# Kernel optimization log

Measured on AMD Instinct MI355X. Metric: run time of the kernel, lower is better.

## Reference

```python
import jax, jax.numpy as jnp
import numpy as np

DIM = 1024
HIDDEN = 2560  # multiple_of*(int(2*4*DIM/3)//multiple_of)
N_EXPERTS = 4
TOP_K = 2


def setup_inputs() -> dict:
    key = jax.random.key(0)
    ks = jax.random.split(key, 5)
    scale_d = 1.0 / np.sqrt(DIM)
    scale_h = 1.0 / np.sqrt(HIDDEN)
    x = jax.random.normal(ks[0], (8, 1024, DIM), dtype=jnp.float32)
    gate_w = jax.random.normal(ks[1], (N_EXPERTS, DIM), dtype=jnp.float32) * scale_d
    # torch Linear weight layout [out, in]; stacked over experts
    w1 = jax.random.normal(ks[2], (N_EXPERTS, HIDDEN, DIM), dtype=jnp.float32) * scale_d
    w3 = jax.random.normal(ks[3], (N_EXPERTS, HIDDEN, DIM), dtype=jnp.float32) * scale_d
    w2 = jax.random.normal(ks[4], (N_EXPERTS, DIM, HIDDEN), dtype=jnp.float32) * scale_h
    return {"x": x, "gate_w": gate_w, "w1": w1, "w2": w2, "w3": w3}


def reference(x, gate_w, w1, w2, w3):
    orig_shape = x.shape
    xf = x.reshape(-1, orig_shape[-1])  # [N, D]

    # gating: softmax -> top-k -> renormalize
    logits = jnp.einsum('nd,ed->ne', xf, gate_w)
    probs = jax.nn.softmax(logits, axis=-1)
    topk_w, topk_idx = jax.lax.top_k(probs, TOP_K)          # [N, K]
    topk_w = topk_w / jnp.sum(topk_w, axis=-1, keepdims=True)

    # per-token per-expert combine weight (0 if expert not selected)
    one_hot = jax.nn.one_hot(topk_idx, N_EXPERTS, dtype=xf.dtype)  # [N, K, E]
    comb = jnp.einsum('nk,nke->ne', topk_w, one_hot)               # [N, E]

    # dense per-expert SwiGLU FFN (4 experts), then weighted combine
    h1 = jnp.einsum('nd,ehd->neh', xf, w1)   # [N, E, H]
    h3 = jnp.einsum('nd,ehd->neh', xf, w3)
    h = jax.nn.silu(h1) * h3
    y = jnp.einsum('neh,edh->ned', h, w2)    # [N, E, D]
    out = jnp.einsum('ned,ne->nd', y, comb)  # [N, D]

    aux_loss = jnp.asarray(0.0, dtype=x.dtype)  # eval mode
    return out.reshape(orig_shape), aux_loss
```

## Files before the change

### kernel.cpp

```cpp
#include <hip/hip_runtime.h>

typedef unsigned short u16;
typedef unsigned int   u32;

#define DIM  1024
#define HID  2560
#define NTOK 8192
#define NEXP 4

#define BM 128
#define BN 128
#define BK 64

#define IDXCAP 16896

typedef __attribute__((ext_vector_type(8))) short bf16x8;
typedef __attribute__((ext_vector_type(4))) float f32x4;

__device__ __forceinline__ void async16(const void* g, void* l) {
  __builtin_amdgcn_global_load_lds((const __attribute__((address_space(1))) u32*)g,
                                   (__attribute__((address_space(3))) u32*)l,
                                   16, 0, 0);
}
__device__ __forceinline__ u16 f2bf(float f) {
  union { float f; u32 u; } c; c.f = f;
  u32 u = c.u;
  return (u16)((u + 0x7fffu + ((u >> 16) & 1u)) >> 16);
}
__device__ __forceinline__ ushort4 cvt4(float4 v) {
  ushort4 o; o.x = f2bf(v.x); o.y = f2bf(v.y); o.z = f2bf(v.z); o.w = f2bf(v.w);
  return o;
}

__global__ void zero_kernel(float* __restrict__ out, int n, int* __restrict__ rt) {
  int i = blockIdx.x * blockDim.x + threadIdx.x;
  if (i < 8) rt[i] = 0;
  int n4 = n >> 2;
  int stride = gridDim.x * blockDim.x;
  float4 z = {0.f, 0.f, 0.f, 0.f};
  for (int j = i; j < n4; j += stride) ((float4*)out)[j] = z;
  if (i == 0)
    for (int j = n4 << 2; j < n; ++j) out[j] = 0.f;
}

__global__ void cvt13_kernel(const float* __restrict__ w1, const float* __restrict__ w3,
                             u16* __restrict__ w1b, u16* __restrict__ w3b, int n4each) {
  int i = blockIdx.x * blockDim.x + threadIdx.x;
  if (i < n4each)
    ((ushort4*)w1b)[i] = cvt4(((const float4*)w1)[i]);
  else if (i < 2 * n4each)
    ((ushort4*)w3b)[i - n4each] = cvt4(((const float4*)w3)[i - n4each]);
}

__global__ void cvt2_kernel(const float* __restrict__ w2, u16* __restrict__ w2b, int n4) {
  int i = blockIdx.x * blockDim.x + threadIdx.x;
  if (i < n4) ((ushort4*)w2b)[i] = cvt4(((const float4*)w2)[i]);
}

__global__ void gate_kernel(const float* __restrict__ X, const float* __restrict__ GW,
                            float* __restrict__ comb, int* __restrict__ rt,
                            u16* __restrict__ Xb) {
  __shared__ int s_cnt[NEXP];
  if (threadIdx.x < NEXP) s_cnt[threadIdx.x] = 0;
  __syncthreads();

  int gtid = blockIdx.x * blockDim.x + threadIdx.x;
  int tok  = gtid >> 6;
  int lane = gtid & 63;

  const float4* xv = (const float4*)(X + (size_t)tok * DIM + lane * 16);
  float4 x0 = xv[0], x1 = xv[1], x2 = xv[2], x3 = xv[3];

  ushort4* xb = (ushort4*)(Xb + (size_t)tok * DIM + lane * 16);
  xb[0] = cvt4(x0); xb[1] = cvt4(x1); xb[2] = cvt4(x2); xb[3] = cvt4(x3);

  float acc[NEXP];
#pragma unroll
  for (int e = 0; e < NEXP; ++e) {
    const float4* gv = (const float4*)(GW + e * DIM + lane * 16);
    float4 g0 = gv[0], g1 = gv[1], g2 = gv[2], g3 = gv[3];
    float s;
    s  = x0.x * g0.x + x0.y * g0.y + x0.z * g0.z + x0.w * g0.w;
    s += x1.x * g1.x + x1.y * g1.y + x1.z * g1.z + x1.w * g1.w;
    s += x2.x * g2.x + x2.y * g2.y + x2.z * g2.z + x2.w * g2.w;
    s += x3.x * g3.x + x3.y * g3.y + x3.z * g3.z + x3.w * g3.w;
    acc[e] = s;
  }
#pragma unroll
  for (int off = 32; off > 0; off >>= 1) {
#pragma unroll
    for (int e = 0; e < NEXP; ++e) acc[e] += __shfl_xor(acc[e], off);
  }
  if (lane == 0) {
    int i1 = 0;
#pragma unroll
    for (int e = 1; e < NEXP; ++e) if (acc[e] > acc[i1]) i1 = e;
    int i2 = -1;
#pragma unroll
    for (int e = 0; e < NEXP; ++e) {
      if (e == i1) continue;
      if (i2 < 0 || acc[e] > acc[i2]) i2 = e;
    }
    float m  = acc[i1];
    float e1 = __expf(acc[i1] - m), e2 = __expf(acc[i2] - m);
    float inv = 1.f / (e1 + e2);
    float w[NEXP] = {0.f, 0.f, 0.f, 0.f};
    w[i1] = e1 * inv; w[i2] = e2 * inv;
#pragma unroll
    for (int e = 0; e < NEXP; ++e) comb[(size_t)tok * NEXP + e] = w[e];
    atomicAdd(&s_cnt[i1], 1);
    atomicAdd(&s_cnt[i2], 1);
  }
  __syncthreads();
  if (threadIdx.x < NEXP) atomicAdd(&rt[threadIdx.x], s_cnt[threadIdx.x]);
}

__global__ void scan_kernel(int* __restrict__ rt) {
  if (threadIdx.x == 0 && blockIdx.x == 0) {
    int b = 0;
#pragma unroll
    for (int e = 0; e < NEXP; ++e) {
      rt[8 + e] = b;
      b += (rt[e] + BM - 1) & ~(BM - 1);
    }
  }
}

__global__ void fill_kernel(const float* __restrict__ comb, int* __restrict__ rt,
                            int* __restrict__ idxpool) {
  int t    = blockIdx.x * blockDim.x + threadIdx.x;
  int lane = threadIdx.x & 63;
  float4 c = ((const float4*)comb)[t];
  float cv[NEXP] = {c.x, c.y, c.z, c.w};
#pragma unroll
  for (int e = 0; e < NEXP; ++e) {
    bool sel = cv[e] > 0.f;
    unsigned long long b = __ballot(sel);
    int cw = __popcll(b);
    int bp = 0;
    if (lane == 0 && cw) bp = atomicAdd(&rt[4 + e], cw);
    bp = __shfl(bp, 0);
    if (sel) {
      int off = __popcll(b & ((1ull << lane) - 1ull));
      idxpool[rt[8 + e] + bp + off] = t;
    }
  }
}


__global__ __launch_bounds__(256, 2) void ffn13_kernel(
    const u16* __restrict__ Xb, const u16* __restrict__ W1,
    const u16* __restrict__ W3, const float* __restrict__ combp,
    const int* __restrict__ idxpool, const int* __restrict__ rt,
    u16* __restrict__ Hpool) {
  const int e   = blockIdx.y >> 6;
  const int mb  = blockIdx.y & 63;
  const int cnt = rt[e];
  const int m0  = mb * BM;
  if (m0 >= cnt) return;
  const int rbase = rt[8 + e];
  const int n0    = blockIdx.x * BN;

  __shared__ __align__(16) u16 As [BM * BK];
  __shared__ __align__(16) u16 B1s[BN * BK];
  __shared__ __align__(16) u16 B3s[BN * BK];
  __shared__ float s_comb[BM];
  __shared__ int   s_idx [BM];

  const int tid  = threadIdx.x;
  const int wave = tid >> 6;
  const int lane = tid & 63;

  if (tid < BM) {
    int m = m0 + tid;
    int t = (m < cnt) ? idxpool[rbase + m] : 0;
    s_idx[tid]  = t;
    s_comb[tid] = combp[(size_t)t * NEXP + e];
  }
  __syncthreads();

  const u16* W1e = W1 + (size_t)e * HID * DIM;
  const u16* W3e = W3 + (size_t)e * HID * DIM;

  const int scc = (((tid & 7) ^ ((tid >> 3) & 7)) << 3);
  const int r0  = tid >> 3;
  const u16 *pA[4], *pB1[4], *pB3[4];
  int dsto[4];
#pragma unroll
  for (int q = 0; q < 4; ++q) {
    int row = r0 + 32 * q;
    pA[q]   = Xb  + (size_t)s_idx[row] * DIM + scc;
    pB1[q]  = W1e + (size_t)(n0 + row) * DIM + scc;
    pB3[q]  = W3e + (size_t)(n0 + row) * DIM + scc;
    dsto[q] = (tid + 256 * q) * 8;
  }

  const int wm = (wave >> 1) * 64, wn = (wave & 1) * 64;
  const int quad = lane >> 4, r = lane & 15;

  f32x4 acc1[4][4], acc3[4][4];
#pragma unroll
  for (int i = 0; i < 4; ++i)
#pragma unroll
    for (int j = 0; j < 4; ++j) {
      acc1[i][j] = (f32x4){0.f, 0.f, 0.f, 0.f};
      acc3[i][j] = (f32x4){0.f, 0.f, 0.f, 0.f};
    }

  for (int k0 = 0; k0 < DIM; k0 += BK) {
    __syncthreads();
#pragma unroll
    for (int q = 0; q < 4; ++q) { async16(pA[q],  &As [dsto[q]]); pA[q]  += BK; }
#pragma unroll
    for (int q = 0; q < 4; ++q) { async16(pB1[q], &B1s[dsto[q]]); pB1[q] += BK; }
#pragma unroll
    for (int q = 0; q < 4; ++q) { async16(pB3[q], &B3s[dsto[q]]); pB3[q] += BK; }
    __syncthreads();

#pragma unroll
    for (int s = 0; s < 2; ++s) {
      bf16x8 af[4], b1f[4], b3f[4];
#pragma unroll
      for (int i = 0; i < 4; ++i) {
        int row = wm + i * 16 + r;
        af[i] = *(const bf16x8*)&As[row * BK + ((((s << 2) + quad) ^ (row & 7)) << 3)];
      }
#pragma unroll
      for (int j = 0; j < 4; ++j) {
        int row = wn + j * 16 + r;
        int cc  = (((s << 2) + quad) ^ (row & 7)) << 3;
        b1f[j] = *(const bf16x8*)&B1s[row * BK + cc];
        b3f[j] = *(const bf16x8*)&B3s[row * BK + cc];
      }
#pragma unroll
      for (int i = 0; i < 4; ++i)
#pragma unroll
        for (int j = 0; j < 4; ++j) {
          acc1[i][j] = __builtin_amdgcn_mfma_f32_16x16x32_bf16(af[i], b1f[j], acc1[i][j], 0, 0, 0);
          acc3[i][j] = __builtin_amdgcn_mfma_f32_16x16x32_bf16(af[i], b3f[j], acc3[i][j], 0, 0, 0);
        }
    }
  }

#pragma unroll
  for (int i = 0; i < 4; ++i) {
    const int rowb = wm + i * 16 + quad * 4;
#pragma unroll
    for (int rr = 0; rr < 4; ++rr) {
      const float cw = s_comb[rowb + rr];
      u16* orow = Hpool + (size_t)(rbase + m0 + rowb + rr) * HID + n0 + wn + r;
#pragma unroll
      for (int j = 0; j < 4; ++j) {
        float v1v = acc1[i][j][rr];
        float v3v = acc3[i][j][rr];
        float sig = 1.f / (1.f + __expf(-v1v));
        orow[j * 16] = f2bf(cw * (v1v * sig * v3v));
      }
    }
  }
}

__global__ __launch_bounds__(256, 2) void ffn2_kernel(
    const u16* __restrict__ Hpool, const u16* __restrict__ W2b,
    const int* __restrict__ idxpool, const int* __restrict__ rt,
    float* __restrict__ Out) {
  const int e   = blockIdx.x >> 9;
  const int bid = blockIdx.x & 511;
  const int cnt = rt[e];
  const int Mb  = (cnt + BM - 1) >> 7;
  const int xcd = bid & 7;
  const int k   = bid >> 3;
  const int mb  = xcd * 8 + (k >> 3);
  const int nb  = k & 7;
  if (mb >= Mb) return;
  const int rbase = rt[8 + e];
  const int m0 = mb * BM;
  const int n0 = nb * BN;

  __shared__ __align__(16) u16 As[BM * BK];
  __shared__ __align__(16) u16 Bs[BN * BK];
  __shared__ int s_idx[BM];

  const int tid  = threadIdx.x;
  const int wave = tid >> 6;
  const int lane = tid & 63;

  if (tid < BM) {
    int m = m0 + tid;
    s_idx[tid] = (m < cnt) ? idxpool[rbase + m] : -1;
  }

  const int scc = (((tid & 7) ^ ((tid >> 3) & 7)) << 3);
  const int r0  = tid >> 3;
  const u16 *pa[4], *pb[4];
  int dsto[4];
#pragma unroll
  for (int q = 0; q < 4; ++q) {
    int row = r0 + 32 * q;
    pa[q]   = Hpool + (size_t)(rbase + m0 + row) * HID + scc;
    pb[q]   = W2b + ((size_t)e * DIM + n0 + row) * HID + scc;
    dsto[q] = (tid + 256 * q) * 8;
  }

  const int wm = (wave >> 1) * 64, wn = (wave & 1) * 64;
  const int quad = lane >> 4, r = lane & 15;

  f32x4 acc[4][4];
#pragma unroll
  for (int i = 0; i < 4; ++i)
#pragma unroll
    for (int j = 0; j < 4; ++j) acc[i][j] = (f32x4){0.f, 0.f, 0.f, 0.f};

  for (int k0 = 0; k0 < HID; k0 += BK) {
    __syncthreads();
#pragma unroll
    for (int q = 0; q < 4; ++q) { async16(pa[q], &As[dsto[q]]); pa[q] += BK; }
#pragma unroll
    for (int q = 0; q < 4; ++q) { async16(pb[q], &Bs[dsto[q]]); pb[q] += BK; }
    __syncthreads();

#pragma unroll
    for (int s = 0; s < 2; ++s) {
      bf16x8 af[4], bf[4];
#pragma unroll
      for (int i = 0; i < 4; ++i) {
        int row = wm + i * 16 + r;
        af[i] = *(const bf16x8*)&As[row * BK + ((((s << 2) + quad) ^ (row & 7)) << 3)];
      }
#pragma unroll
      for (int j = 0; j < 4; ++j) {
        int row = wn + j * 16 + r;
        bf[j] = *(const bf16x8*)&Bs[row * BK + ((((s << 2) + quad) ^ (row & 7)) << 3)];
      }
#pragma unroll
      for (int i = 0; i < 4; ++i)
#pragma unroll
        for (int j = 0; j < 4; ++j)
          acc[i][j] = __builtin_amdgcn_mfma_f32_16x16x32_bf16(af[i], bf[j], acc[i][j], 0, 0, 0);
    }
  }

#pragma unroll
  for (int i = 0; i < 4; ++i) {
    const int rowb = wm + i * 16 + quad * 4;
#pragma unroll
    for (int rr = 0; rr < 4; ++rr) {
      int t = s_idx[rowb + rr];
      if (t >= 0) {
        float* orow = Out + (size_t)t * DIM + n0 + wn + r;
#pragma unroll
        for (int j = 0; j < 4; ++j) unsafeAtomicAdd(&orow[j * 16], acc[i][j][rr]);
      }
    }
  }
}

__global__ void ws_marker_kernel(float* __restrict__ Out, float v) {
  if (threadIdx.x == 0 && blockIdx.x == 0) Out[0] = v;
}

extern "C" void kernel_launch(void* const* d_in, const int* in_sizes, int n_in,
                              void* d_out, int out_size, void* d_ws, size_t ws_size,
                              hipStream_t stream) {
  const float* x  = (const float*)d_in[0];
  const float* gw = (const float*)d_in[1];
  const float* w1 = (const float*)d_in[2];
  const float* w2 = (const float*)d_in[3];
  const float* w3 = (const float*)d_in[4];
  float* out = (float*)d_out;

  const size_t WELEMS = (size_t)NEXP * HID * DIM;
  const size_t WBYTES = WELEMS * sizeof(u16);
  char* ws = (char*)d_ws;
  float* comb    = (float*)ws;
  int*   rt      = (int*)(ws + 131072);
  int*   idxpool = (int*)(ws + 131072 + 128);
  u16*   w1b     = (u16*)(ws + 131072 + 128 + (size_t)IDXCAP * 4);
  u16*   w2b     = w1b;
  u16*   w3b     = w1b + WELEMS;
  u16*   Xb      = w3b + WELEMS;
  u16*   Hpool   = Xb + (size_t)NTOK * DIM;

  const size_t need = 131072 + 128 + (size_t)IDXCAP * 4 + 2 * WBYTES +
                      (size_t)NTOK * DIM * sizeof(u16) +
                      (size_t)IDXCAP * HID * sizeof(u16);
  if (ws_size < need) {
    float v = 5000.0f + (float)((ws_size >> 20) > 999 ? 999 : (ws_size >> 20));
    ws_marker_kernel<<<dim3(1), dim3(64), 0, stream>>>(out, v);
    return;
  }

  zero_kernel<<<dim3(2048), dim3(256), 0, stream>>>(out, out_size / 4, rt);

  gate_kernel<<<dim3(NTOK / 4), dim3(256), 0, stream>>>(x, gw, comb, rt, Xb);
  scan_kernel<<<dim3(1), dim3(64), 0, stream>>>(rt);
  fill_kernel<<<dim3(NTOK / 256), dim3(256), 0, stream>>>(comb, rt, idxpool);

  {
    int n4each = (int)(WELEMS / 4);
    cvt13_kernel<<<dim3((2 * n4each + 255) / 256), dim3(256), 0, stream>>>(
        w1, w3, w1b, w3b, n4each);
  }

  ffn13_kernel<<<dim3(HID / BN, 64 * NEXP), dim3(256), 0, stream>>>(
      Xb, w1b, w3b, comb, idxpool, rt, Hpool);

  {
    int n4 = (int)(WELEMS / 4);
    cvt2_kernel<<<dim3((n4 + 255) / 256), dim3(256), 0, stream>>>(w2, w2b, n4);
  }

  ffn2_kernel<<<dim3(512 * NEXP), dim3(256), 0, stream>>>(Hpool, w2b, idxpool, rt, out);
}
```

Measured before the change: 567.6 us.

## Fuse zeroing and scan into other kernels; compact ffn2 grid to active tiles

Moves the output zeroing into the gate kernel and the routing-counter reset into the w1/w3 conversion kernel. It replaces the scan kernel with an inline per-expert base computation, which removes two kernel launches. ffn2 becomes a grid-stride loop over only the tiles that are actually populated, so blocks that would exit early on empty tiles are no longer launched. Each thread now recomputes expert offsets, and tile ordering changes from the XCD-aware mapping to an mb-major order, which may affect L2 reuse.

Result: faster. 522.8 us (-7.9%).

```diff
diff --git a/kernel.cpp b/kernel.cpp
--- a/kernel.cpp
+++ b/kernel.cpp
@@ -31,20 +31,20 @@
   ushort4 o; o.x = f2bf(v.x); o.y = f2bf(v.y); o.z = f2bf(v.z); o.w = f2bf(v.w);
   return o;
 }
-
-__global__ void zero_kernel(float* __restrict__ out, int n, int* __restrict__ rt) {
-  int i = blockIdx.x * blockDim.x + threadIdx.x;
-  if (i < 8) rt[i] = 0;
-  int n4 = n >> 2;
-  int stride = gridDim.x * blockDim.x;
-  float4 z = {0.f, 0.f, 0.f, 0.f};
-  for (int j = i; j < n4; j += stride) ((float4*)out)[j] = z;
-  if (i == 0)
-    for (int j = n4 << 2; j < n; ++j) out[j] = 0.f;
+__device__ __forceinline__ int ebase(const int* __restrict__ rt, int e) {
+  int b = 0;
+#pragma unroll
+  for (int q = 0; q < NEXP; ++q) {
+    int p = (rt[q] + BM - 1) & ~(BM - 1);
+    if (q < e) b += p;
+  }
+  return b;
 }
 
 __global__ void cvt13_kernel(const float* __restrict__ w1, const float* __restrict__ w3,
-                             u16* __restrict__ w1b, u16* __restrict__ w3b, int n4each) {
+                             u16* __restrict__ w1b, u16* __restrict__ w3b, int n4each,
+                             int* __restrict__ rt) {
+  if (blockIdx.x == 0 && threadIdx.x < 8) rt[threadIdx.x] = 0;
   int i = blockIdx.x * blockDim.x + threadIdx.x;
   if (i < n4each)
     ((ushort4*)w1b)[i] = cvt4(((const float4*)w1)[i]);
@@ -59,12 +59,22 @@
 
 __global__ void gate_kernel(const float* __restrict__ X, const float* __restrict__ GW,
                             float* __restrict__ comb, int* __restrict__ rt,
-                            u16* __restrict__ Xb) {
+                            u16* __restrict__ Xb, float* __restrict__ out, int out_n) {
   __shared__ int s_cnt[NEXP];
   if (threadIdx.x < NEXP) s_cnt[threadIdx.x] = 0;
+
+  int gtid = blockIdx.x * blockDim.x + threadIdx.x;
+
+  {
+    int n4 = out_n >> 2;
+    int stride = gridDim.x * blockDim.x;
+    float4 z = {0.f, 0.f, 0.f, 0.f};
+    for (int j = gtid; j < n4; j += stride) ((float4*)out)[j] = z;
+    if (gtid == 0)
+      for (int j = n4 << 2; j < out_n; ++j) out[j] = 0.f;
+  }
   __syncthreads();
 
-  int gtid = blockIdx.x * blockDim.x + threadIdx.x;
   int tok  = gtid >> 6;
   int lane = gtid & 63;
 
@@ -115,17 +125,6 @@
   if (threadIdx.x < NEXP) atomicAdd(&rt[threadIdx.x], s_cnt[threadIdx.x]);
 }
 
-__global__ void scan_kernel(int* __restrict__ rt) {
-  if (threadIdx.x == 0 && blockIdx.x == 0) {
-    int b = 0;
-#pragma unroll
-    for (int e = 0; e < NEXP; ++e) {
-      rt[8 + e] = b;
-      b += (rt[e] + BM - 1) & ~(BM - 1);
-    }
-  }
-}
-
 __global__ void fill_kernel(const float* __restrict__ comb, int* __restrict__ rt,
                             int* __restrict__ idxpool) {
   int t    = blockIdx.x * blockDim.x + threadIdx.x;
@@ -142,7 +141,7 @@
     bp = __shfl(bp, 0);
     if (sel) {
       int off = __popcll(b & ((1ull << lane) - 1ull));
-      idxpool[rt[8 + e] + bp + off] = t;
+      idxpool[ebase(rt, e) + bp + off] = t;
     }
   }
 }
@@ -158,7 +157,7 @@
   const int cnt = rt[e];
   const int m0  = mb * BM;
   if (m0 >= cnt) return;
-  const int rbase = rt[8 + e];
+  const int rbase = ebase(rt, e);
   const int n0    = blockIdx.x * BN;
 
   __shared__ __align__(16) u16 As [BM * BK];
@@ -264,92 +263,105 @@
     const u16* __restrict__ Hpool, const u16* __restrict__ W2b,
     const int* __restrict__ idxpool, const int* __restrict__ rt,
     float* __restrict__ Out) {
-  const int e   = blockIdx.x >> 9;
-  const int bid = blockIdx.x & 511;
-  const int cnt = rt[e];
-  const int Mb  = (cnt + BM - 1) >> 7;
-  const int xcd = bid & 7;
-  const int k   = bid >> 3;
-  const int mb  = xcd * 8 + (k >> 3);
-  const int nb  = k & 7;
-  if (mb >= Mb) return;
-  const int rbase = rt[8 + e];
-  const int m0 = mb * BM;
-  const int n0 = nb * BN;
-
   __shared__ __align__(16) u16 As[BM * BK];
   __shared__ __align__(16) u16 Bs[BN * BK];
   __shared__ int s_idx[BM];
 
+  int cnt_[NEXP], Mb_[NEXP], base_[NEXP], rb_[NEXP];
+  int total = 0, rb = 0;
+#pragma unroll
+  for (int e = 0; e < NEXP; ++e) {
+    cnt_[e]  = rt[e];
+    Mb_[e]   = (cnt_[e] + BM - 1) >> 7;
+    base_[e] = total;
+    rb_[e]   = rb;
+    total   += Mb_[e] * (DIM / BN);
+    rb      += (cnt_[e] + BM - 1) & ~(BM - 1);
+  }
+
   const int tid  = threadIdx.x;
   const int wave = tid >> 6;
   const int lane = tid & 63;
-
-  if (tid < BM) {
-    int m = m0 + tid;
-    s_idx[tid] = (m < cnt) ? idxpool[rbase + m] : -1;
-  }
-
-  const int scc = (((tid & 7) ^ ((tid >> 3) & 7)) << 3);
-  const int r0  = tid >> 3;
-  const u16 *pa[4], *pb[4];
-  int dsto[4];
-#pragma unroll
-  for (int q = 0; q < 4; ++q) {
-    int row = r0 + 32 * q;
-    pa[q]   = Hpool + (size_t)(rbase + m0 + row) * HID + scc;
-    pb[q]   = W2b + ((size_t)e * DIM + n0 + row) * HID + scc;
-    dsto[q] = (tid + 256 * q) * 8;
-  }
-
+  const int scc  = (((tid & 7) ^ ((tid >> 3) & 7)) << 3);
+  const int r0   = tid >> 3;
   const int wm = (wave >> 1) * 64, wn = (wave & 1) * 64;
   const int quad = lane >> 4, r = lane & 15;
 
-  f32x4 acc[4][4];
-#pragma unroll
-  for (int i = 0; i < 4; ++i)
-#pragma unroll
-    for (int j = 0; j < 4; ++j) acc[i][j] = (f32x4){0.f, 0.f, 0.f, 0.f};
-
-  for (int k0 = 0; k0 < HID; k0 += BK) {
+  for (int t = blockIdx.x; t < total; t += gridDim.x) {
+    int e = 0;
+#pragma unroll
+    for (int q = 1; q < NEXP; ++q) if (t >= base_[q]) e = q;
+    const int tl  = t - base_[e];
+    const int Mb  = Mb_[e];
+    const int mb  = tl % Mb;
+    const int nb  = tl / Mb;
+    const int cnt = cnt_[e];
+    const int rbase = rb_[e];
+    const int m0 = mb * BM;
+    const int n0 = nb * BN;
+
     __syncthreads();
-#pragma unroll
-    for (int q = 0; q < 4; ++q) { async16(pa[q], &As[dsto[q]]); pa[q] += BK; }
-#pragma unroll
-    for (int q = 0; q < 4; ++q) { async16(pb[q], &Bs[dsto[q]]); pb[q] += BK; }
-    __syncthreads();
-
-#pragma unroll
-    for (int s = 0; s < 2; ++s) {
-      bf16x8 af[4], bf[4];
-#pragma unroll
-      for (int i = 0; i < 4; ++i) {
-        int row = wm + i * 16 + r;
-        af[i] = *(const bf16x8*)&As[row * BK + ((((s << 2) + quad) ^ (row & 7)) << 3)];
+    if (tid < BM) {
+      int m = m0 + tid;
+      s_idx[tid] = (m < cnt) ? idxpool[rbase + m] : -1;
+    }
+
+    const u16 *pa[4], *pb[4];
+    int dsto[4];
+#pragma unroll
+    for (int q = 0; q < 4; ++q) {
+      int row = r0 + 32 * q;
+      pa[q]   = Hpool + (size_t)(rbase + m0 + row) * HID + scc;
+      pb[q]   = W2b + ((size_t)e * DIM + n0 + row) * HID + scc;
+      dsto[q] = (tid + 256 * q) * 8;
+    }
+
+    f32x4 acc[4][4];
+#pragma unroll
+    for (int i = 0; i < 4; ++i)
+#pragma unroll
+      for (int j = 0; j < 4; ++j) acc[i][j] = (f32x4){0.f, 0.f, 0.f, 0.f};
+
+    for (int k0 = 0; k0 < HID; k0 += BK) {
+      __syncthreads();
+#pragma unroll
+      for (int q = 0; q < 4; ++q) { async16(pa[q], &As[dsto[q]]); pa[q] += BK; }
+#pragma unroll
+      for (int q = 0; q < 4; ++q) { async16(pb[q], &Bs[dsto[q]]); pb[q] += BK; }
+      __syncthreads();
+
+#pragma unroll
+      for (int s = 0; s < 2; ++s) {
+        bf16x8 af[4], bf[4];
+#pragma unroll
+        for (int i = 0; i < 4; ++i) {
+          int row = wm + i * 16 + r;
+          af[i] = *(const bf16x8*)&As[row * BK + ((((s << 2) + quad) ^ (row & 7)) << 3)];
+        }
+#pragma unroll
+        for (int j = 0; j < 4; ++j) {
+          int row = wn + j * 16 + r;
+          bf[j] = *(const bf16x8*)&Bs[row * BK + ((((s << 2) + quad) ^ (row & 7)) << 3)];
+        }
+#pragma unroll
+        for (int i = 0; i < 4; ++i)
+#pragma unroll
+          for (int j = 0; j < 4; ++j)
+            acc[i][j] = __builtin_amdgcn_mfma_f32_16x16x32_bf16(af[i], bf[j], acc[i][j], 0, 0, 0);
       }
-#pragma unroll
-      for (int j = 0; j < 4; ++j) {
-        int row = wn + j * 16 + r;
-        bf[j] = *(const bf16x8*)&Bs[row * BK + ((((s << 2) + quad) ^ (row & 7)) << 3)];
-      }
-#pragma unroll
-      for (int i = 0; i < 4; ++i)
-#pragma unroll
-        for (int j = 0; j < 4; ++j)
-          acc[i][j] = __builtin_amdgcn_mfma_f32_16x16x32_bf16(af[i], bf[j], acc[i][j], 0, 0, 0);
-    }
-  }
-
-#pragma unroll
-  for (int i = 0; i < 4; ++i) {
-    const int rowb = wm + i * 16 + quad * 4;
-#pragma unroll
-    for (int rr = 0; rr < 4; ++rr) {
-      int t = s_idx[rowb + rr];
-      if (t >= 0) {
-        float* orow = Out + (size_t)t * DIM + n0 + wn + r;
-#pragma unroll
-        for (int j = 0; j < 4; ++j) unsafeAtomicAdd(&orow[j * 16], acc[i][j][rr]);
+    }
+
+#pragma unroll
+    for (int i = 0; i < 4; ++i) {
+      const int rowb = wm + i * 16 + quad * 4;
+#pragma unroll
+      for (int rr = 0; rr < 4; ++rr) {
+        int tk = s_idx[rowb + rr];
+        if (tk >= 0) {
+          float* orow = Out + (size_t)tk * DIM + n0 + wn + r;
+#pragma unroll
+          for (int j = 0; j < 4; ++j) unsafeAtomicAdd(&orow[j * 16], acc[i][j][rr]);
+        }
       }
     }
   }
@@ -390,17 +402,15 @@
     return;
   }
 
-  zero_kernel<<<dim3(2048), dim3(256), 0, stream>>>(out, out_size / 4, rt);
-
-  gate_kernel<<<dim3(NTOK / 4), dim3(256), 0, stream>>>(x, gw, comb, rt, Xb);
-  scan_kernel<<<dim3(1), dim3(64), 0, stream>>>(rt);
-  fill_kernel<<<dim3(NTOK / 256), dim3(256), 0, stream>>>(comb, rt, idxpool);
-
   {
     int n4each = (int)(WELEMS / 4);
     cvt13_kernel<<<dim3((2 * n4each + 255) / 256), dim3(256), 0, stream>>>(
-        w1, w3, w1b, w3b, n4each);
-  }
+        w1, w3, w1b, w3b, n4each, rt);
+  }
+
+  gate_kernel<<<dim3(NTOK / 4), dim3(256), 0, stream>>>(x, gw, comb, rt, Xb,
+                                                        out, out_size / 4);
+  fill_kernel<<<dim3(NTOK / 256), dim3(256), 0, stream>>>(comb, rt, idxpool);
 
   ffn13_kernel<<<dim3(HID / BN, 64 * NEXP), dim3(256), 0, stream>>>(
       Xb, w1b, w3b, comb, idxpool, rt, Hpool);
@@ -410,5 +420,5 @@
     cvt2_kernel<<<dim3((n4 + 255) / 256), dim3(256), 0, stream>>>(w2, w2b, n4);
   }
 
-  ffn2_kernel<<<dim3(512 * NEXP), dim3(256), 0, stream>>>(Hpool, w2b, idxpool, rt, out);
-}
+  ffn2_kernel<<<dim3(2048), dim3(256), 0, stream>>>(Hpool, w2b, idxpool, rt, out);
+}
```
